# Kernel optimization log

Hardware: AMD Instinct MI355X
Metric: run time of the kernel (lower is better)

Reference implementation:

```python
import jax, jax.numpy as jnp
import numpy as np

N = 50000      # nodes
E = 800000     # edges
IN_DIM = 16
D = 128        # latent_dim == d_model == num_heads*d_head
H = 8
DH = 16
DFF = 512
L = 3          # n_layers
CLAMP = 5.0
EPS = 1e-5


def _layer_norm(x, g, b):
    mu = jnp.mean(x, axis=-1, keepdims=True)
    var = jnp.mean((x - mu) ** 2, axis=-1, keepdims=True)
    return (x - mu) * jax.lax.rsqrt(var + EPS) * g + b


def setup_inputs() -> dict:
    key = jax.random.key(0)
    ks = jax.random.split(key, 16)
    def w(k, shape, fan_in):
        return jax.random.normal(k, shape, dtype=jnp.float32) * (1.0 / np.sqrt(fan_in))
    inp = {
        "nf": jax.random.normal(ks[0], (N, IN_DIM), dtype=jnp.float32),
        "src": jax.random.randint(ks[1], (E,), 0, N, dtype=jnp.int32),
        "dst": jax.random.randint(ks[2], (E,), 0, N, dtype=jnp.int32),
        "enc_W": w(ks[3], (D, IN_DIM), IN_DIM),
        "enc_b": jnp.zeros((D,), jnp.float32),
        "Wq": w(ks[4], (L, H * DH, D), D),
        "Wk": w(ks[5], (L, H * DH, D), D),
        "Wv": w(ks[6], (L, H * DH, D), D),
        "Wo": w(ks[7], (L, D, H * DH), H * DH),
        "ln1_g": jnp.ones((L, D), jnp.float32),
        "ln1_b": jnp.zeros((L, D), jnp.float32),
        "ffn_W1": w(ks[8], (L, DFF, D), D),
        "ffn_b1": jnp.zeros((L, DFF), jnp.float32),
        "ffn_W2": w(ks[9], (L, D, DFF), DFF),
        "ffn_b2": jnp.zeros((L, D), jnp.float32),
        "ln2_g": jnp.ones((L, D), jnp.float32),
        "ln2_b": jnp.zeros((L, D), jnp.float32),
        "dec_W": w(ks[10], (1, D), D),
        "dec_b": jnp.zeros((1,), jnp.float32),
    }
    return inp


def reference(nf, src, dst, enc_W, enc_b, Wq, Wk, Wv, Wo, ln1_g, ln1_b,
              ffn_W1, ffn_b1, ffn_W2, ffn_b2, ln2_g, ln2_b, dec_W, dec_b):
    h = nf @ enc_W.T + enc_b                       # [N, D]
    scale = 1.0 / np.sqrt(DH)
    for l in range(L):
        q = h @ Wq[l].T                            # [N, H*DH]
        k = h @ Wk[l].T
        v = h @ Wv[l].T
        qe = q[dst].reshape(E, H, DH)              # per-edge gather (dst query)
        ke = k[src].reshape(E, H, DH)
        u = jnp.sum(qe * ke, axis=-1) * scale      # [E, H]
        u = jnp.clip(u, -CLAMP, CLAMP)
        # edge_softmax: normalize over edges sharing the same dst node
        m = jax.ops.segment_max(u, dst, num_segments=N)   # [N, H]
        e = jnp.exp(u - m[dst])
        s = jax.ops.segment_sum(e, dst, num_segments=N)   # [N, H]
        a = e / s[dst]                             # [E, H]
        av = a[..., None] * v[src].reshape(E, H, DH)      # [E, H, DH]
        sum_av = jax.ops.segment_sum(av.reshape(E, H * DH), dst, num_segments=N)
        uh = sum_av @ Wo[l].T                      # [N, D]
        h1 = _layer_norm(h + uh, ln1_g[l], ln1_b[l])
        f = jax.nn.relu(h1 @ ffn_W1[l].T + ffn_b1[l]) @ ffn_W2[l].T + ffn_b2[l]
        h = _layer_norm(h1 + f, ln2_g[l], ln2_b[l])
    pred = h @ dec_W.T + dec_b                     # [N, 1]
    # BasicReadout('mean') over the single batched graph -> [1, 1]
    return jnp.mean(pred, axis=0, keepdims=True)
```

## Files before the change

kernel.cpp:

```cpp
#include <hip/hip_runtime.h>
#include <math.h>

static constexpr int D   = 128;
static constexpr int DFF = 512;
static constexpr int LAYERS = 3;
static constexpr float CLAMP_V = 5.0f;
static constexpr float LN_EPS = 1e-5f;

typedef unsigned short u16;
typedef unsigned int   u32;
typedef short bf16x8 __attribute__((ext_vector_type(8)));
typedef float f32x4  __attribute__((ext_vector_type(4)));

__device__ inline float4 ld4(const float* p){ return *reinterpret_cast<const float4*>(p); }
__device__ inline u16 f2bf(float f){ u32 u = __float_as_uint(f); return (u16)((u + 0x7fff + ((u>>16)&1)) >> 16); }
__device__ inline float bl(u32 u){ return __uint_as_float(u << 16); }
__device__ inline float bh(u32 u){ return __uint_as_float(u & 0xffff0000u); }

__device__ inline void gload_lds16(const void* g, void* l) {
  __builtin_amdgcn_global_load_lds(
      (const __attribute__((address_space(1))) void*)g,
      (__attribute__((address_space(3))) void*)l, 16, 0, 0);
}

__global__ __launch_bounds__(256) void count_kernel(const int* __restrict__ dst,
                                                    int* __restrict__ deg, int E)
{
  int e = blockIdx.x*256 + threadIdx.x;
  if (e < E) atomicAdd(&deg[dst[e]], 1);
}

__global__ __launch_bounds__(256) void scan_bsum(const int* __restrict__ deg,
                                                 int* __restrict__ bsum, int N)
{
  const int i0 = blockIdx.x*1024 + threadIdx.x*4;
  int s = 0;
  if (i0 + 3 < N) { int4 v = *(const int4*)&deg[i0]; s = v.x+v.y+v.z+v.w; }
  else { for (int t = 0; t < 4; t++) if (i0+t < N) s += deg[i0+t]; }
  #pragma unroll
  for (int off = 1; off < 64; off <<= 1) s += __shfl_xor(s, off);
  __shared__ int ws_[4];
  if ((threadIdx.x & 63) == 0) ws_[threadIdx.x >> 6] = s;
  __syncthreads();
  if (threadIdx.x == 0) bsum[blockIdx.x] = ws_[0]+ws_[1]+ws_[2]+ws_[3];
}

__global__ __launch_bounds__(64) void scan_bbase(int* __restrict__ bsum, int NB)
{
  const int tid = threadIdx.x;
  int base = 0;
  for (int c = 0; c < NB; c += 64) {
    const int idx = c + tid;
    int v = (idx < NB) ? bsum[idx] : 0;
    const int orig = v;
    #pragma unroll
    for (int off = 1; off < 64; off <<= 1) {
      int t = __shfl_up(v, off);
      if (tid >= off) v += t;
    }
    if (idx < NB) bsum[idx] = base + v - orig;
    base += __shfl(v, 63);
  }
}

__global__ __launch_bounds__(256) void scan_write(const int* __restrict__ deg,
    const int* __restrict__ bbase, int* __restrict__ offs, int* __restrict__ cursor, int N)
{
  const int i0 = blockIdx.x*1024 + threadIdx.x*4;
  int v[4] = {0,0,0,0};
  if (i0 + 3 < N) { int4 t = *(const int4*)&deg[i0]; v[0]=t.x; v[1]=t.y; v[2]=t.z; v[3]=t.w; }
  else { for (int t = 0; t < 4; t++) if (i0+t < N) v[t] = deg[i0+t]; }
  const int s = v[0]+v[1]+v[2]+v[3];
  const int lane = threadIdx.x & 63, w = threadIdx.x >> 6;
  int inc = s;
  #pragma unroll
  for (int off = 1; off < 64; off <<= 1) {
    int t = __shfl_up(inc, off);
    if (lane >= off) inc += t;
  }
  __shared__ int wsum[4];
  if (lane == 63) wsum[w] = inc;
  __syncthreads();
  int wb = 0;
  for (int t = 0; t < 4; t++) if (t < w) wb += wsum[t];
  int run = bbase[blockIdx.x] + wb + inc - s;
  #pragma unroll
  for (int t = 0; t < 4; t++) {
    if (i0 + t < N) { offs[i0+t] = run; cursor[i0+t] = run; run += v[t]; }
  }
  if (i0 <= N-1 && N-1 < i0+4) offs[N] = run;
}

__global__ __launch_bounds__(256) void fill_kernel(const int* __restrict__ dst,
    const int* __restrict__ src, int* __restrict__ cursor, int* __restrict__ csr_src, int E)
{
  int e = blockIdx.x*256 + threadIdx.x;
  if (e < E) {
    int p = atomicAdd(&cursor[dst[e]], 1);
    csr_src[p] = src[e];
  }
}

__global__ __launch_bounds__(256) void convert_weights(
    const float* __restrict__ Wq, const float* __restrict__ Wk, const float* __restrict__ Wv,
    const float* __restrict__ Wo, const float* __restrict__ W1, const float* __restrict__ W2,
    u16* __restrict__ out)
{
  const int SQKV = 3*384*128;
  const int SWO  = 3*128*128;
  const int SW1  = 3*512*128;
  const int SW2  = 3*128*512;
  int i = blockIdx.x*256 + threadIdx.x;
  if (i >= SQKV+SWO+SW1+SW2) return;
  float v;
  if (i < SQKV) {
    int l = i / (384*128), rem = i % (384*128);
    int row = rem / 128, col = rem % 128;
    const float* W = (row < 128) ? Wq : ((row < 256) ? Wk : Wv);
    v = W[(size_t)l*128*128 + (size_t)(row & 127)*128 + col];
  } else if (i < SQKV+SWO) {
    v = Wo[i - SQKV];
  } else if (i < SQKV+SWO+SW1) {
    v = W1[i - SQKV - SWO];
  } else {
    v = W2[i - SQKV - SWO - SW1];
  }
  out[i] = f2bf(v);
}

__global__ __launch_bounds__(256) void encoder_kernel(
    const float* __restrict__ nf, const float* __restrict__ W,
    const float* __restrict__ b, float* __restrict__ h, u16* __restrict__ hb, int N)
{
  int n = blockIdx.x*2 + (threadIdx.x >> 7);
  int d = threadIdx.x & 127;
  if (n >= N) return;
  const float* nr = nf + (size_t)n*16;
  const float* wr = W  + (size_t)d*16;
  float s = b[d];
  #pragma unroll
  for (int kk = 0; kk < 16; kk++) s = fmaf(nr[kk], wr[kk], s);
  h[(size_t)n*D + d]  = s;
  hb[(size_t)n*D + d] = f2bf(s);
}

__device__ inline void mfma_step128(const u16* __restrict__ la, const u16* __restrict__ lb,
                                    int lane, int wr, int wc, f32x4 (&acc)[4][4])
{
  #pragma unroll
  for (int k2 = 0; k2 < 2; k2++) {
    bf16x8 af[4], bfr[4];
    const int kq = k2*4 + (lane >> 4);
    #pragma unroll
    for (int mi = 0; mi < 4; mi++) {
      const int r = wr*64 + mi*16 + (lane & 15);
      af[mi] = *(const bf16x8*)&la[r*64 + ((kq ^ (r & 7)) << 3)];
    }
    #pragma unroll
    for (int ni = 0; ni < 4; ni++) {
      const int r = wc*64 + ni*16 + (lane & 15);
      bfr[ni] = *(const bf16x8*)&lb[r*64 + ((kq ^ (r & 7)) << 3)];
    }
    #pragma unroll
    for (int mi = 0; mi < 4; mi++)
      #pragma unroll
      for (int ni = 0; ni < 4; ni++)
        acc[mi][ni] = __builtin_amdgcn_mfma_f32_16x16x32_bf16(af[mi], bfr[ni], acc[mi][ni], 0, 0, 0);
  }
}

__device__ inline void mfma_stage64(const u16* __restrict__ Atile, const u16* __restrict__ Btile,
                                    int lane, int wr, int wc, int kabase, f32x4 (&acc)[2][4])
{
  #pragma unroll
  for (int k2 = 0; k2 < 2; k2++) {
    const int kql = k2*4 + (lane >> 4);
    const int kqa = kabase + kql;
    bf16x8 af[2], bfr[4];
    #pragma unroll
    for (int mi = 0; mi < 2; mi++) {
      const int r = wr*32 + mi*16 + (lane & 15);
      const int slot = ((kqa & 7) ^ (r & 7)) | (kqa & 8);
      af[mi] = *(const bf16x8*)&Atile[r*128 + slot*8];
    }
    #pragma unroll
    for (int ni = 0; ni < 4; ni++) {
      const int r = wc*64 + ni*16 + (lane & 15);
      bfr[ni] = *(const bf16x8*)&Btile[r*64 + ((kql ^ (r & 7)) << 3)];
    }
    #pragma unroll
    for (int mi = 0; mi < 2; mi++)
      #pragma unroll
      for (int ni = 0; ni < 4; ni++)
        acc[mi][ni] = __builtin_amdgcn_mfma_f32_16x16x32_bf16(af[mi], bfr[ni], acc[mi][ni], 0, 0, 0);
  }
}

__global__ __launch_bounds__(256) void gemm_qkv(
    const u16* __restrict__ A, const u16* __restrict__ B,
    float* __restrict__ qf, u16* __restrict__ kvb, int M)
{
  __shared__ u16 lA[2][128*64];
  __shared__ u16 lW[2][128*64];
  const int m0 = blockIdx.x * 128;
  const int tid = threadIdx.x, lane = tid & 63, wid = tid >> 6;
  const int wr = wid >> 1, wc = wid & 1;
  const int ldrow = lane >> 3;
  const int gran  = (lane & 7) ^ ldrow;

  auto issueA = [&](int ks) {
    const int k0 = ks*64 + gran*8;
    #pragma unroll
    for (int is = 0; is < 4; is++) {
      const int r = wid*32 + is*8;
      int gm = m0 + r + ldrow; if (gm >= M) gm = M - 1;
      gload_lds16(A + (size_t)gm*128 + k0, &lA[ks][r*64]);
    }
  };
  auto issueW = [&](int s) {
    const u16* Bm = B + (size_t)(s >> 1)*128*128;
    const int k0 = (s & 1)*64 + gran*8;
    #pragma unroll
    for (int is = 0; is < 4; is++) {
      const int r = wid*32 + is*8;
      gload_lds16(Bm + (size_t)(r + ldrow)*128 + k0, &lW[s & 1][r*64]);
    }
  };

  issueA(0); issueA(1); issueW(0); issueW(1);
  asm volatile("s_waitcnt vmcnt(4)" ::: "memory");
  __builtin_amdgcn_s_barrier();

  f32x4 acc[4][4];
  const int rbase = m0 + wr*64 + ((lane >> 4) << 2);
  const int cbase = wc*64 + (lane & 15);

  #pragma unroll
  for (int s = 0; s < 6; s++) {
    if ((s & 1) == 0) {
      #pragma unroll
      for (int i = 0; i < 4; i++)
        #pragma unroll
        for (int j = 0; j < 4; j++) { acc[i][j][0]=0.f; acc[i][j][1]=0.f; acc[i][j][2]=0.f; acc[i][j][3]=0.f; }
    }
    mfma_step128(lA[s & 1], lW[s & 1], lane, wr, wc, acc);
    if (s & 1) {
      const int mat = s >> 1;
      #pragma unroll
      for (int ni = 0; ni < 4; ni++) {
        const int col = cbase + ni*16;
        #pragma unroll
        for (int mi = 0; mi < 4; mi++) {
          #pragma unroll
          for (int r = 0; r < 4; r++) {
            const int gm = rbase + mi*16 + r;
            if (gm < M) {
              if (mat == 0) qf[(size_t)gm*128 + col] = acc[mi][ni][r];
              else          kvb[(size_t)gm*256 + (mat-1)*128 + col] = f2bf(acc[mi][ni][r]);
            }
          }
        }
      }
    }
    if (s < 5) {
      asm volatile("s_waitcnt lgkmcnt(0)" ::: "memory");
      __builtin_amdgcn_s_barrier();
      if (s < 4) issueW(s + 2);
      if (s == 4) { asm volatile("s_waitcnt vmcnt(0)" ::: "memory"); }
      else        { asm volatile("s_waitcnt vmcnt(4)" ::: "memory"); }
      __builtin_amdgcn_s_barrier();
    }
  }
}

__global__ __launch_bounds__(256) void ffn_fused(
    const u16* __restrict__ savb, const u16* __restrict__ Wo,
    const u16* __restrict__ W1,   const u16* __restrict__ W2,
    const float* __restrict__ ln1g, const float* __restrict__ ln1b,
    const float* __restrict__ b1,   const float* __restrict__ b2,
    const float* __restrict__ ln2g, const float* __restrict__ ln2b,
    float* __restrict__ hf, u16* __restrict__ hb, int M)
{
  __shared__ u16 lB[2][128*64];
  __shared__ u16 h1s[64*128];
  __shared__ u16 fs[64*128];
  __shared__ float lsum[64][2];
  __shared__ float lsq[64][2];

  const int tid  = threadIdx.x;
  const int lane = tid & 63;
  const int wid  = tid >> 6;
  const int wr   = wid >> 1, wc = wid & 1;
  const int m0   = blockIdx.x * 64;

  const int ldrow = lane >> 3;
  const int gran  = (lane & 7) ^ ldrow;

  const int rbase_l = wr*32 + ((lane >> 4) << 2);
  const int cbase   = wc*64 + (lane & 15);

  auto stage_issue = [&](int s) {
    u16* dst = lB[s & 1];
    #pragma unroll
    for (int is = 0; is < 4; is++) {
      const int r = wid*32 + is*8;
      const u16* gp;
      if (s < 2) gp = Wo + (size_t)(r + ldrow)*128 + s*64;
      else {
        const int t = s - 2, c = t >> 2, k = t & 3;
        gp = (k < 2) ? (W1 + (size_t)(c*128 + r + ldrow)*128 + k*64)
                     : (W2 + (size_t)(r + ldrow)*512 + c*128 + (k-2)*64);
      }
      gload_lds16(gp + gran*8, dst + r*64);
    }
  };

  #pragma unroll
  for (int is = 0; is < 4; is++) {
    const int r0 = wid*16 + is*4;
    const int rr = r0 + (lane >> 4);
    int gm = m0 + rr; if (gm >= M) gm = M - 1;
    const int gsrc = ((lane & 7) ^ (rr & 7)) | (lane & 8);
    gload_lds16(savb + (size_t)gm*128 + gsrc*8, &fs[r0*128]);
  }
  stage_issue(0);
  stage_issue(1);
  asm volatile("s_waitcnt vmcnt(4)" ::: "memory");
  __builtin_amdgcn_s_barrier();

  f32x4 acc1[2][4], acc2[2][4], acc3[2][4];
  #pragma unroll
  for (int i = 0; i < 2; i++)
    #pragma unroll
    for (int j = 0; j < 4; j++) {
      acc1[i][j][0]=0.f; acc1[i][j][1]=0.f; acc1[i][j][2]=0.f; acc1[i][j][3]=0.f;
      acc3[i][j][0]=0.f; acc3[i][j][1]=0.f; acc3[i][j][2]=0.f; acc3[i][j][3]=0.f;
    }

  #pragma unroll
  for (int s = 0; s < 18; s++) {
    if (s >= 2 && ((s - 2) & 3) == 0) {
      #pragma unroll
      for (int i = 0; i < 2; i++)
        #pragma unroll
        for (int j = 0; j < 4; j++) { acc2[i][j][0]=0.f; acc2[i][j][1]=0.f; acc2[i][j][2]=0.f; acc2[i][j][3]=0.f; }
    }

    if (s < 2)
      mfma_stage64(fs,  lB[s & 1], lane, wr, wc, (s & 1)*8, acc1);
    else if (((s - 2) & 3) < 2)
      mfma_stage64(h1s, lB[s & 1], lane, wr, wc, (s & 1)*8, acc2);
    else
      mfma_stage64(fs,  lB[s & 1], lane, wr, wc, (s & 1)*8, acc3);

    if (s == 1) {
      #pragma unroll
      for (int mi = 0; mi < 2; mi++) {
        #pragma unroll
        for (int r = 0; r < 4; r++) {
          const int lrow = rbase_l + mi*16 + r;
          int gr = m0 + lrow; if (gr >= M) gr = M - 1;
          float ps = 0.f, pq = 0.f;
          #pragma unroll
          for (int ni = 0; ni < 4; ni++) {
            const int col = cbase + ni*16;
            float x = acc1[mi][ni][r] + hf[(size_t)gr*128 + col];
            acc1[mi][ni][r] = x;
            ps += x; pq += x*x;
          }
          #pragma unroll
          for (int off = 1; off < 16; off <<= 1) { ps += __shfl_xor(ps, off); pq += __shfl_xor(pq, off); }
          if ((lane & 15) == 0) { lsum[lrow][wc] = ps; lsq[lrow][wc] = pq; }
        }
      }
      __syncthreads();
      #pragma unroll
      for (int mi = 0; mi < 2; mi++) {
        #pragma unroll
        for (int r = 0; r < 4; r++) {
          const int lrow = rbase_l + mi*16 + r;
          const float mean = (lsum[lrow][0] + lsum[lrow][1]) * (1.0f/128.0f);
          float var = (lsq[lrow][0] + lsq[lrow][1]) * (1.0f/128.0f) - mean*mean;
          const float rstd = rsqrtf(fmaxf(var, 0.f) + LN_EPS);
          #pragma unroll
          for (int ni = 0; ni < 4; ni++) {
            const int col = cbase + ni*16;
            float o = (acc1[mi][ni][r] - mean) * rstd * ln1g[col] + ln1b[col];
            acc1[mi][ni][r] = o;
            const int g16 = col >> 3;
            const int slot = ((g16 & 7) ^ (lrow & 7)) | (g16 & 8);
            h1s[lrow*128 + slot*8 + (col & 7)] = f2bf(o);
          }
        }
      }
    } else if (s >= 2 && ((s - 2) & 3) == 1) {
      const int c = (s - 2) >> 2;
      #pragma unroll
      for (int mi = 0; mi < 2; mi++) {
        #pragma unroll
        for (int r = 0; r < 4; r++) {
          const int lrow = rbase_l + mi*16 + r;
          #pragma unroll
          for (int ni = 0; ni < 4; ni++) {
            const int col = cbase + ni*16;
            float v = fmaxf(acc2[mi][ni][r] + b1[c*128 + col], 0.f);
            const int g16 = col >> 3;
            const int slot = ((g16 & 7) ^ (lrow & 7)) | (g16 & 8);
            fs[lrow*128 + slot*8 + (col & 7)] = f2bf(v);
          }
        }
      }
    }

    if (s < 17) {
      asm volatile("s_waitcnt lgkmcnt(0)" ::: "memory");
      __builtin_amdgcn_s_barrier();
      if (s < 16) stage_issue(s + 2);
      if (s == 16) { asm volatile("s_waitcnt vmcnt(0)" ::: "memory"); }
      else         { asm volatile("s_waitcnt vmcnt(4)" ::: "memory"); }
      __builtin_amdgcn_s_barrier();
    }
  }

  #pragma unroll
  for (int mi = 0; mi < 2; mi++) {
    #pragma unroll
    for (int r = 0; r < 4; r++) {
      const int lrow = rbase_l + mi*16 + r;
      float ps = 0.f, pq = 0.f;
      #pragma unroll
      for (int ni = 0; ni < 4; ni++) {
        const int col = cbase + ni*16;
        float x = acc3[mi][ni][r] + b2[col] + acc1[mi][ni][r];
        acc3[mi][ni][r] = x;
        ps += x; pq += x*x;
      }
      #pragma unroll
      for (int off = 1; off < 16; off <<= 1) { ps += __shfl_xor(ps, off); pq += __shfl_xor(pq, off); }
      if ((lane & 15) == 0) { lsum[lrow][wc] = ps; lsq[lrow][wc] = pq; }
    }
  }
  __syncthreads();
  #pragma unroll
  for (int mi = 0; mi < 2; mi++) {
    #pragma unroll
    for (int r = 0; r < 4; r++) {
      const int lrow = rbase_l + mi*16 + r;
      const int grow = m0 + lrow;
      if (grow >= M) continue;
      const float mean = (lsum[lrow][0] + lsum[lrow][1]) * (1.0f/128.0f);
      float var = (lsq[lrow][0] + lsq[lrow][1]) * (1.0f/128.0f) - mean*mean;
      const float rstd = rsqrtf(fmaxf(var, 0.f) + LN_EPS);
      #pragma unroll
      for (int ni = 0; ni < 4; ni++) {
        const int col = cbase + ni*16;
        float o = (acc3[mi][ni][r] - mean) * rstd * ln2g[col] + ln2b[col];
        hf[(size_t)grow*128 + col] = o;
        hb[(size_t)grow*128 + col] = f2bf(o);
      }
    }
  }
}

__global__ __launch_bounds__(256) void attn_kernel(
    const float* __restrict__ q, const u16* __restrict__ kv,
    const int* __restrict__ offs, const int* __restrict__ csr_src,
    u16* __restrict__ outb, int N)
{
  const int tid = threadIdx.x;
  const int j   = tid & 15;
  const int n   = blockIdx.x*16 + (tid >> 4);
  if (n >= N) return;

  float qreg[8];
  *(float4*)&qreg[0] = ld4(&q[(size_t)n*128 + j*8]);
  *(float4*)&qreg[4] = ld4(&q[(size_t)n*128 + j*8 + 4]);

  const int start = offs[n];
  const int deg   = offs[n+1] - start;

  float s = 0.f;
  float acc[8] = {0,0,0,0,0,0,0,0};
  const int gb = tid & 48;

  for (int base = 0; base < deg; base += 16) {
    const int myidx = base + j;
    const int sn_mine = (myidx < deg) ? csr_src[start + myidx] : 0;
    const int cnt = (deg - base < 16) ? (deg - base) : 16;

    for (int b2 = 0; b2 < cnt; b2 += 8) {
      const int m8 = cnt - b2;
      uint4 K4[8], V4[8];
      #pragma unroll
      for (int u = 0; u < 8; u++) {
        const int sel = b2 + ((u < m8) ? u : 0);
        const int sn = __shfl(sn_mine, gb + sel);
        const u16* row = kv + (size_t)sn*256 + j*8;
        K4[u] = *(const uint4*)row;
        V4[u] = *(const uint4*)(row + 128);
      }
      #pragma unroll
      for (int u = 0; u < 8; u++) {
        if (u < m8) {
          float d = bl(K4[u].x)*qreg[0] + bh(K4[u].x)*qreg[1]
                  + bl(K4[u].y)*qreg[2] + bh(K4[u].y)*qreg[3]
                  + bl(K4[u].z)*qreg[4] + bh(K4[u].z)*qreg[5]
                  + bl(K4[u].w)*qreg[6] + bh(K4[u].w)*qreg[7];
          d += __shfl_xor(d, 1);
          float uu = fminf(fmaxf(d * 0.25f, -CLAMP_V), CLAMP_V);
          float e = __expf(uu - CLAMP_V);
          s += e;
          acc[0] = fmaf(e, bl(V4[u].x), acc[0]);
          acc[1] = fmaf(e, bh(V4[u].x), acc[1]);
          acc[2] = fmaf(e, bl(V4[u].y), acc[2]);
          acc[3] = fmaf(e, bh(V4[u].y), acc[3]);
          acc[4] = fmaf(e, bl(V4[u].z), acc[4]);
          acc[5] = fmaf(e, bh(V4[u].z), acc[5]);
          acc[6] = fmaf(e, bl(V4[u].w), acc[6]);
          acc[7] = fmaf(e, bh(V4[u].w), acc[7]);
        }
      }
    }
  }

  const float rs = (deg > 0) ? (1.0f / s) : 0.f;
  u16 o[8];
  #pragma unroll
  for (int t = 0; t < 8; t++) o[t] = f2bf(acc[t] * rs);
  *(uint4*)&outb[(size_t)n*128 + j*8] = *(const uint4*)o;
}

__global__ __launch_bounds__(256) void dec_partial(const float* __restrict__ h,
    const float* __restrict__ W, float* __restrict__ partials, int N)
{
  float acc = 0.f;
  for (int n = blockIdx.x*256 + threadIdx.x; n < N; n += 256*256) {
    const float* hr = h + (size_t)n*D;
    float s = 0.f;
    #pragma unroll
    for (int t = 0; t < 32; t++) {
      float4 hv = ld4(&hr[t*4]); float4 wv = ld4(&W[t*4]);
      s += hv.x*wv.x + hv.y*wv.y + hv.z*wv.z + hv.w*wv.w;
    }
    acc += s;
  }
  #pragma unroll
  for (int off = 1; off < 64; off <<= 1) acc += __shfl_xor(acc, off);
  __shared__ float red[4];
  int lane = threadIdx.x & 63, w = threadIdx.x >> 6;
  if (lane == 0) red[w] = acc;
  __syncthreads();
  if (threadIdx.x == 0) partials[blockIdx.x] = red[0]+red[1]+red[2]+red[3];
}

__global__ __launch_bounds__(256) void dec_final(const float* __restrict__ partials,
    const float* __restrict__ decb, float* __restrict__ out, int N)
{
  float a = partials[threadIdx.x];
  #pragma unroll
  for (int off = 1; off < 64; off <<= 1) a += __shfl_xor(a, off);
  __shared__ float red[4];
  int lane = threadIdx.x & 63, w = threadIdx.x >> 6;
  if (lane == 0) red[w] = a;
  __syncthreads();
  if (threadIdx.x == 0) out[0] = (red[0]+red[1]+red[2]+red[3]) / (float)N + decb[0];
}

extern "C" void kernel_launch(void* const* d_in, const int* in_sizes, int n_in,
                              void* d_out, int out_size, void* d_ws, size_t ws_size,
                              hipStream_t stream)
{
  const float* nf   = (const float*)d_in[0];
  const int*   src  = (const int*)  d_in[1];
  const int*   dst  = (const int*)  d_in[2];
  const float* encW = (const float*)d_in[3];
  const float* encb = (const float*)d_in[4];
  const float* Wq   = (const float*)d_in[5];
  const float* Wk   = (const float*)d_in[6];
  const float* Wv   = (const float*)d_in[7];
  const float* Wo   = (const float*)d_in[8];
  const float* ln1g = (const float*)d_in[9];
  const float* ln1b = (const float*)d_in[10];
  const float* W1   = (const float*)d_in[11];
  const float* b1   = (const float*)d_in[12];
  const float* W2   = (const float*)d_in[13];
  const float* b2   = (const float*)d_in[14];
  const float* ln2g = (const float*)d_in[15];
  const float* ln2b = (const float*)d_in[16];
  const float* decW = (const float*)d_in[17];
  const float* decb = (const float*)d_in[18];
  float* out = (float*)d_out;

  const int N = in_sizes[0] / 16;
  const int E = in_sizes[1];
  const int NB = (N + 1023) / 1024;

  float* ws   = (float*)d_ws;
  float* h    = ws;
  float* q    = h  + (size_t)N*128;
  u16*  hb    = (u16*)(q + (size_t)N*128);
  u16*  kvb   = hb  + (size_t)N*128;
  u16*  savb  = kvb + (size_t)N*256;
  int* deg    = (int*)(savb + (size_t)N*128);
  int* offs   = deg + N;
  int* cursor = offs + N + 1;
  int* csr    = cursor + N;
  int* bsum   = csr + E;
  float* partials = (float*)(bsum + ((NB + 255) & ~255));
  u16* wbuf   = (u16*)(partials + 512);
  u16* wqkv   = wbuf;
  u16* wo_b   = wbuf + 147456;
  u16* w1_b   = wbuf + 196608;
  u16* w2_b   = wbuf + 393216;

  hipMemsetAsync(deg, 0, sizeof(int)*N, stream);
  count_kernel<<<(E+255)/256, 256, 0, stream>>>(dst, deg, E);
  scan_bsum<<<NB, 256, 0, stream>>>(deg, bsum, N);
  scan_bbase<<<1, 64, 0, stream>>>(bsum, NB);
  scan_write<<<NB, 256, 0, stream>>>(deg, bsum, offs, cursor, N);
  fill_kernel<<<(E+255)/256, 256, 0, stream>>>(dst, src, cursor, csr, E);

  convert_weights<<<(589824+255)/256, 256, 0, stream>>>(Wq, Wk, Wv, Wo, W1, W2, wbuf);

  encoder_kernel<<<(N+1)/2, 256, 0, stream>>>(nf, encW, encb, h, hb, N);

  const int gmx = (N + 127)/128;
  for (int l = 0; l < LAYERS; l++) {
    const u16* wqkv_l = wqkv + (size_t)l*384*128;
    const u16* wo_l   = wo_b + (size_t)l*128*128;
    const u16* w1_l   = w1_b + (size_t)l*512*128;
    const u16* w2_l   = w2_b + (size_t)l*128*512;

    gemm_qkv<<<gmx, 256, 0, stream>>>(hb, wqkv_l, q, kvb, N);

    attn_kernel<<<(N+15)/16, 256, 0, stream>>>(q, kvb, offs, csr, savb, N);

    ffn_fused<<<(N+63)/64, 256, 0, stream>>>(
        savb, wo_l, w1_l, w2_l,
        ln1g + l*D, ln1b + l*D, b1 + l*DFF, b2 + l*D, ln2g + l*D, ln2b + l*D,
        h, hb, N);
  }

  dec_partial<<<256, 256, 0, stream>>>(h, decW, partials, N);
  dec_final<<<1, 256, 0, stream>>>(partials, decb, out, N);
}
```

Baseline: 541.3 us.

## Fuse edge attention into the FFN kernel and drop the savb round trip

```diff
diff --git a/kernel.cpp b/kernel.cpp
--- a/kernel.cpp
+++ b/kernel.cpp
@@ -273,8 +273,10 @@
   }
 }
 
-__global__ __launch_bounds__(256) void ffn_fused(
-    const u16* __restrict__ savb, const u16* __restrict__ Wo,
+__global__ __launch_bounds__(256) void attn_ffn(
+    const float* __restrict__ q, const u16* __restrict__ kv,
+    const int* __restrict__ offs, const int* __restrict__ csr_src,
+    const u16* __restrict__ Wo,
     const u16* __restrict__ W1,   const u16* __restrict__ W2,
     const float* __restrict__ ln1g, const float* __restrict__ ln1b,
     const float* __restrict__ b1,   const float* __restrict__ b2,
@@ -315,18 +317,75 @@
     }
   };
 
-  #pragma unroll
-  for (int is = 0; is < 4; is++) {
-    const int r0 = wid*16 + is*4;
-    const int rr = r0 + (lane >> 4);
-    int gm = m0 + rr; if (gm >= M) gm = M - 1;
-    const int gsrc = ((lane & 7) ^ (rr & 7)) | (lane & 8);
-    gload_lds16(savb + (size_t)gm*128 + gsrc*8, &fs[r0*128]);
-  }
   stage_issue(0);
   stage_issue(1);
-  asm volatile("s_waitcnt vmcnt(4)" ::: "memory");
-  __builtin_amdgcn_s_barrier();
+
+  {
+    const int j  = tid & 15;
+    const int gb = tid & 48;
+    #pragma unroll 1
+    for (int p = 0; p < 4; p++) {
+      const int lr = p*16 + (tid >> 4);
+      const int n  = m0 + lr;
+      float s = 0.f;
+      float acc[8] = {0,0,0,0,0,0,0,0};
+      if (n < M) {
+        float qreg[8];
+        *(float4*)&qreg[0] = ld4(&q[(size_t)n*128 + j*8]);
+        *(float4*)&qreg[4] = ld4(&q[(size_t)n*128 + j*8 + 4]);
+        const int start = offs[n];
+        const int deg   = offs[n+1] - start;
+        for (int base = 0; base < deg; base += 16) {
+          const int myidx = base + j;
+          const int sn_mine = (myidx < deg) ? csr_src[start + myidx] : 0;
+          const int cnt = (deg - base < 16) ? (deg - base) : 16;
+          for (int b2 = 0; b2 < cnt; b2 += 8) {
+            const int m8 = cnt - b2;
+            uint4 K4[8], V4[8];
+            #pragma unroll
+            for (int u = 0; u < 8; u++) {
+              const int sel = b2 + ((u < m8) ? u : 0);
+              const int sn = __shfl(sn_mine, gb + sel);
+              const u16* row = kv + (size_t)sn*256 + j*8;
+              K4[u] = *(const uint4*)row;
+              V4[u] = *(const uint4*)(row + 128);
+            }
+            #pragma unroll
+            for (int u = 0; u < 8; u++) {
+              if (u < m8) {
+                float d = bl(K4[u].x)*qreg[0] + bh(K4[u].x)*qreg[1]
+                        + bl(K4[u].y)*qreg[2] + bh(K4[u].y)*qreg[3]
+                        + bl(K4[u].z)*qreg[4] + bh(K4[u].z)*qreg[5]
+                        + bl(K4[u].w)*qreg[6] + bh(K4[u].w)*qreg[7];
+                d += __shfl_xor(d, 1);
+                float uu = fminf(fmaxf(d * 0.25f, -CLAMP_V), CLAMP_V);
+                float e = __expf(uu - CLAMP_V);
+                s += e;
+                acc[0] = fmaf(e, bl(V4[u].x), acc[0]);
+                acc[1] = fmaf(e, bh(V4[u].x), acc[1]);
+                acc[2] = fmaf(e, bl(V4[u].y), acc[2]);
+                acc[3] = fmaf(e, bh(V4[u].y), acc[3]);
+                acc[4] = fmaf(e, bl(V4[u].z), acc[4]);
+                acc[5] = fmaf(e, bh(V4[u].z), acc[5]);
+                acc[6] = fmaf(e, bl(V4[u].w), acc[6]);
+                acc[7] = fmaf(e, bh(V4[u].w), acc[7]);
+              }
+            }
+          }
+        }
+        const float rs = (deg > 0) ? (1.0f / s) : 0.f;
+        #pragma unroll
+        for (int t = 0; t < 8; t++) acc[t] *= rs;
+      }
+      u16 o[8];
+      #pragma unroll
+      for (int t = 0; t < 8; t++) o[t] = f2bf(acc[t]);
+      const int slot = ((j & 7) ^ (lr & 7)) | (j & 8);
+      *(uint4*)&fs[lr*128 + slot*8] = *(const uint4*)o;
+    }
+  }
+  asm volatile("s_waitcnt vmcnt(0)" ::: "memory");
+  __syncthreads();
 
   f32x4 acc1[2][4], acc2[2][4], acc3[2][4];
   #pragma unroll
@@ -460,74 +519,6 @@
       }
     }
   }
-}
-
-__global__ __launch_bounds__(256) void attn_kernel(
-    const float* __restrict__ q, const u16* __restrict__ kv,
-    const int* __restrict__ offs, const int* __restrict__ csr_src,
-    u16* __restrict__ outb, int N)
-{
-  const int tid = threadIdx.x;
-  const int j   = tid & 15;
-  const int n   = blockIdx.x*16 + (tid >> 4);
-  if (n >= N) return;
-
-  float qreg[8];
-  *(float4*)&qreg[0] = ld4(&q[(size_t)n*128 + j*8]);
-  *(float4*)&qreg[4] = ld4(&q[(size_t)n*128 + j*8 + 4]);
-
-  const int start = offs[n];
-  const int deg   = offs[n+1] - start;
-
-  float s = 0.f;
-  float acc[8] = {0,0,0,0,0,0,0,0};
-  const int gb = tid & 48;
-
-  for (int base = 0; base < deg; base += 16) {
-    const int myidx = base + j;
-    const int sn_mine = (myidx < deg) ? csr_src[start + myidx] : 0;
-    const int cnt = (deg - base < 16) ? (deg - base) : 16;
-
-    for (int b2 = 0; b2 < cnt; b2 += 8) {
-      const int m8 = cnt - b2;
-      uint4 K4[8], V4[8];
-      #pragma unroll
-      for (int u = 0; u < 8; u++) {
-        const int sel = b2 + ((u < m8) ? u : 0);
-        const int sn = __shfl(sn_mine, gb + sel);
-        const u16* row = kv + (size_t)sn*256 + j*8;
-        K4[u] = *(const uint4*)row;
-        V4[u] = *(const uint4*)(row + 128);
-      }
-      #pragma unroll
-      for (int u = 0; u < 8; u++) {
-        if (u < m8) {
-          float d = bl(K4[u].x)*qreg[0] + bh(K4[u].x)*qreg[1]
-                  + bl(K4[u].y)*qreg[2] + bh(K4[u].y)*qreg[3]
-                  + bl(K4[u].z)*qreg[4] + bh(K4[u].z)*qreg[5]
-                  + bl(K4[u].w)*qreg[6] + bh(K4[u].w)*qreg[7];
-          d += __shfl_xor(d, 1);
-          float uu = fminf(fmaxf(d * 0.25f, -CLAMP_V), CLAMP_V);
-          float e = __expf(uu - CLAMP_V);
-          s += e;
-          acc[0] = fmaf(e, bl(V4[u].x), acc[0]);
-          acc[1] = fmaf(e, bh(V4[u].x), acc[1]);
-          acc[2] = fmaf(e, bl(V4[u].y), acc[2]);
-          acc[3] = fmaf(e, bh(V4[u].y), acc[3]);
-          acc[4] = fmaf(e, bl(V4[u].z), acc[4]);
-          acc[5] = fmaf(e, bh(V4[u].z), acc[5]);
-          acc[6] = fmaf(e, bl(V4[u].w), acc[6]);
-          acc[7] = fmaf(e, bh(V4[u].w), acc[7]);
-        }
-      }
-    }
-  }
-
-  const float rs = (deg > 0) ? (1.0f / s) : 0.f;
-  u16 o[8];
-  #pragma unroll
-  for (int t = 0; t < 8; t++) o[t] = f2bf(acc[t] * rs);
-  *(uint4*)&outb[(size_t)n*128 + j*8] = *(const uint4*)o;
 }
 
 __global__ __launch_bounds__(256) void dec_partial(const float* __restrict__ h,
@@ -600,8 +591,7 @@
   float* q    = h  + (size_t)N*128;
   u16*  hb    = (u16*)(q + (size_t)N*128);
   u16*  kvb   = hb  + (size_t)N*128;
-  u16*  savb  = kvb + (size_t)N*256;
-  int* deg    = (int*)(savb + (size_t)N*128);
+  int* deg    = (int*)(kvb + (size_t)N*256);
   int* offs   = deg + N;
   int* cursor = offs + N + 1;
   int* csr    = cursor + N;
@@ -625,6 +615,7 @@
   encoder_kernel<<<(N+1)/2, 256, 0, stream>>>(nf, encW, encb, h, hb, N);
 
   const int gmx = (N + 127)/128;
+  const int g64 = (N + 63)/64;
   for (int l = 0; l < LAYERS; l++) {
     const u16* wqkv_l = wqkv + (size_t)l*384*128;
     const u16* wo_l   = wo_b + (size_t)l*128*128;
@@ -633,10 +624,8 @@
 
     gemm_qkv<<<gmx, 256, 0, stream>>>(hb, wqkv_l, q, kvb, N);
 
-    attn_kernel<<<(N+15)/16, 256, 0, stream>>>(q, kvb, offs, csr, savb, N);
-
-    ffn_fused<<<(N+63)/64, 256, 0, stream>>>(
-        savb, wo_l, w1_l, w2_l,
+    attn_ffn<<<g64, 256, 0, stream>>>(
+        q, kvb, offs, csr, wo_l, w1_l, w2_l,
         ln1g + l*D, ln1b + l*D, b1 + l*DFF, b2 + l*D, ln2g + l*D, ln2b + l*D,
         h, hb, N);
   }
```

Result: no change. 547.0 us (+1.1%).
